# Optimization experiments

Hardware: AMD Instinct MI355X
Metric: run time of the kernel (lower is better)

The kernel has to match this reference:

```python
import jax, jax.numpy as jnp
import numpy as np

NFEAT, NHID, NHEADS = 512, 64, 8
ALPHA = 0.2
NEG = -9e15  # torch uses -9000000000000000.0


def _xavier(key, shape, gain=1.414):
    fan_in, fan_out = shape[-2], shape[-1]
    bound = gain * np.sqrt(6.0 / (fan_in + fan_out))
    return jax.random.uniform(key, shape, jnp.float32, -bound, bound)


def setup_inputs() -> dict:
    key = jax.random.key(0)
    ks = jax.random.split(key, 6)
    N = 2048
    x = jax.random.normal(ks[0], (N, NFEAT), jnp.float32)
    adj = jax.random.randint(ks[1], (N, N), 0, 2, jnp.int32)
    # per-head stacked params for the two attention banks
    W1 = _xavier(ks[2], (NHEADS, NFEAT, NHID))
    a1 = _xavier(ks[3], (NHEADS, 2 * NHID, 1))
    W2 = _xavier(ks[4], (NHEADS, NFEAT, NHID))
    a2 = _xavier(ks[5], (NHEADS, 2 * NHID, 1))
    return {"x": x, "adj": adj, "W1": W1, "a1": a1, "W2": W2, "a2": a2}


def _gat_bank(x, adj_mask, W, a):
    """All heads of one GraphAttentionLayer bank, vectorized over heads.
    x: [N, F], W: [H, F, O], a: [H, 2O, 1]. Returns concat output [N, H*O]
    and attention [H, N, N]."""
    N = x.shape[0]
    Wh = jnp.einsum('nf,hfo->hno', x, W)               # [H, N, O]
    a_src = a[:, :NHID, 0]                             # [H, O]
    a_dst = a[:, NHID:, 0]                             # [H, O]
    Wh1 = jnp.einsum('hno,ho->hn', Wh, a_src)          # [H, N]
    Wh2 = jnp.einsum('hno,ho->hn', Wh, a_dst)          # [H, N]
    e = Wh1[:, :, None] + Wh2[:, None, :]              # [H, N, N]
    e = jnp.where(e > 0, e, ALPHA * e)                 # LeakyReLU
    e = jnp.where(adj_mask[None, :, :], e, NEG)
    attention = jax.nn.softmax(e, axis=-1)             # [H, N, N]
    h_prime = jnp.einsum('hnm,hmo->hno', attention, Wh)
    out = jax.nn.elu(h_prime)                          # concat=True -> elu
    # torch.cat over heads along feature dim: [N, H*O]
    out = jnp.transpose(out, (1, 0, 2)).reshape(N, NHEADS * NHID)
    return out, attention


def reference(x, adj, W1, a1, W2, a2):
    adj_mask = adj > 0
    # dropout layers are no-ops in eval mode
    h1, att1 = _gat_bank(x, adj_mask, W1, a1)
    h1 = jax.nn.elu(h1)
    h2, att2 = _gat_bank(h1, adj_mask, W2, a2)
    h2 = jax.nn.elu(h2)
    return h2, att1, att2
```

## Files before the change

kernel.cpp:

```cpp
#include <hip/hip_runtime.h>
#include <hip/hip_bf16.h>


typedef __attribute__((ext_vector_type(8))) short bf16x8;
typedef __attribute__((ext_vector_type(4))) float f32x4;

__device__ __forceinline__ float bf2f(unsigned short u) {
    return __uint_as_float(((unsigned int)u) << 16);
}
__device__ __forceinline__ unsigned short f2bf(float f) {
    __hip_bfloat16 h = __float2bfloat16(f);
    return __builtin_bit_cast(unsigned short, h);
}
__device__ __forceinline__ float elu1(float x) { return x > 0.f ? x : expm1f(x); }

__global__ __launch_bounds__(256) void adjbits_kernel(
    const int* __restrict__ adj, unsigned long long* __restrict__ gbits) {
    int g = blockIdx.x * 256 + threadIdx.x;
    unsigned long long m = __ballot(adj[g] > 0);
    if ((threadIdx.x & 63) == 0) gbits[g >> 6] = m;
}

__global__ __launch_bounds__(256) void reorder_w_kernel(
    const float* __restrict__ W, unsigned short* __restrict__ WpHi,
    unsigned short* __restrict__ WpLo) {
    int i = blockIdx.x * 256 + threadIdx.x;
    int o = i & 63;
    int k = (i >> 6) & 511;
    int h = i >> 15;
    float v = W[i];
    unsigned short hi = f2bf(v);
    unsigned short lo = f2bf(v - bf2f(hi));
    long idx = (((h * 16) + (k >> 5)) * 64 + o) * 32 + (k & 31);
    WpHi[idx] = hi;
    WpLo[idx] = lo;
}

__global__ __launch_bounds__(256, 2) void gemm1_kernel(
    const float* __restrict__ A,
    const unsigned short* __restrict__ BpHi, const unsigned short* __restrict__ BpLo,
    const float* __restrict__ avec,
    unsigned short* __restrict__ Whp, float* __restrict__ s1, float* __restrict__ s2) {
    __shared__ float accred[2][64][20];
    const int bx   = blockIdx.x;
    const int h    = bx >> 6;
    const int mt   = bx & 63;
    const int tid  = threadIdx.x;
    const int wave = tid >> 6;
    const int lane = tid & 63;
    const int quad = lane >> 4;
    const int m16  = lane & 15;
    const int rw   = wave & 1;
    const int kw   = wave >> 1;
    const int rowbase = mt * 32 + rw * 16;

    const float* Arow = A + (long)(rowbase + m16) * 512 + kw * 256 + quad * 8;
    const long boff = ((long)(h * 16 + kw * 8) * 64 + m16) * 32 + quad * 8;
    const unsigned short* BH = BpHi + boff;
    const unsigned short* BL = BpLo + boff;

    f32x4 acc[4];
#pragma unroll
    for (int t = 0; t < 4; ++t)
#pragma unroll
        for (int r = 0; r < 4; ++r) acc[t][r] = 0.f;

    for (int kb = 0; kb < 8; ++kb) {
        const float* ap = Arow + kb * 32;
        bf16x8 ahi, alo;
#pragma unroll
        for (int j = 0; j < 8; ++j) {
            float v = ap[j];
            unsigned short hv = f2bf(v);
            ahi[j] = (short)hv;
            alo[j] = (short)f2bf(v - bf2f(hv));
        }
        const unsigned short* bh0 = BH + (long)kb * 2048;
        const unsigned short* bl0 = BL + (long)kb * 2048;
#pragma unroll
        for (int t = 0; t < 4; ++t) {
            bf16x8 bh = *reinterpret_cast<const bf16x8*>(bh0 + t * 512);
            bf16x8 bl = *reinterpret_cast<const bf16x8*>(bl0 + t * 512);
            acc[t] = __builtin_amdgcn_mfma_f32_16x16x32_bf16(alo, bh, acc[t], 0, 0, 0);
            acc[t] = __builtin_amdgcn_mfma_f32_16x16x32_bf16(ahi, bl, acc[t], 0, 0, 0);
            acc[t] = __builtin_amdgcn_mfma_f32_16x16x32_bf16(ahi, bh, acc[t], 0, 0, 0);
        }
    }

    if (kw == 1) {
#pragma unroll
        for (int t = 0; t < 4; ++t)
            *reinterpret_cast<f32x4*>(&accred[rw][t * 16 + m16][quad * 4]) = acc[t];
    }
    __syncthreads();
    if (kw == 1) return;

#pragma unroll
    for (int t = 0; t < 4; ++t) {
        f32x4 o = *reinterpret_cast<const f32x4*>(&accred[rw][t * 16 + m16][quad * 4]);
#pragma unroll
        for (int r = 0; r < 4; ++r) acc[t][r] += o[r];
    }

    float aS[4], aD[4];
#pragma unroll
    for (int t = 0; t < 4; ++t) {
        aS[t] = avec[(h << 7) + t * 16 + m16];
        aD[t] = avec[(h << 7) + 64 + t * 16 + m16];
    }
#pragma unroll
    for (int r = 0; r < 4; ++r) {
        float t1 = 0.f, t2 = 0.f;
#pragma unroll
        for (int t = 0; t < 4; ++t) {
            float v = acc[t][r];
            t1 = fmaf(v, aS[t], t1);
            t2 = fmaf(v, aD[t], t2);
        }
#pragma unroll
        for (int off = 1; off < 16; off <<= 1) {
            t1 += __shfl_xor(t1, off);
            t2 += __shfl_xor(t2, off);
        }
        if (m16 == 0) {
            int row = rowbase + quad * 4 + r;
            s1[(h << 11) + row] = t1;
            s2[(h << 11) + row] = t2;
        }
    }

#pragma unroll
    for (int t = 0; t < 4; ++t) {
        const int col = t * 16 + m16;
#pragma unroll
        for (int r = 0; r < 4; ++r) {
            const int row = rowbase + quad * 4 + r;
            long idx = (((long)(h * 64 + (row >> 5)) * 64 + col) << 5) + (row & 31);
            Whp[idx] = f2bf(acc[t][r]);
        }
    }
}

__global__ __launch_bounds__(256, 4) void fused_att_kernel(
    const float* __restrict__ s1g, const float* __restrict__ s2g,
    const unsigned int* __restrict__ gbits,
    const unsigned short* __restrict__ Whp,
    float* __restrict__ att, float* __restrict__ hout) {
    __shared__ unsigned int lbits[16 * 65];
    __shared__ float ls2[2048];
    __shared__ float lmax[4][16];
    __shared__ float lsum[4][16];
    __shared__ float accred[3][64][20];
    __shared__ f32x4 pstage[4][16][9];

    const int bx   = blockIdx.x;
    const int h    = bx >> 7;
    const int row0 = (bx & 127) << 4;
    const int tid  = threadIdx.x;
    const int wq   = tid >> 6;
    const int lane = tid & 63;
    const int quad = lane >> 4;
    const int m16  = lane & 15;

#pragma unroll
    for (int i = 0; i < 4; ++i) {
        int idx = i * 256 + tid;
        lbits[(idx >> 6) * 65 + (idx & 63)] = gbits[((row0 + (idx >> 6)) << 6) + (idx & 63)];
    }
    const float4* s2v4 = reinterpret_cast<const float4*>(s2g + (h << 11));
#pragma unroll
    for (int i = 0; i < 2; ++i) {
        int idx = i * 256 + tid;
        reinterpret_cast<float4*>(ls2)[idx] = s2v4[idx];
    }
    __syncthreads();

    const float s1i = s1g[(h << 11) + row0 + m16];

    float mx = -INFINITY;
    float lp = 0.f;
    for (int i = 0; i < 16; ++i) {
        const int jt = i * 4 + wq;
        unsigned int word = lbits[m16 * 65 + jt] >> (quad * 8);
        float4 sa = *reinterpret_cast<const float4*>(ls2 + jt * 32 + quad * 8);
        float4 sb = *reinterpret_cast<const float4*>(ls2 + jt * 32 + quad * 8 + 4);
        float sv[8] = {sa.x, sa.y, sa.z, sa.w, sb.x, sb.y, sb.z, sb.w};
        float ev[8];
        float bm = -INFINITY;
#pragma unroll
        for (int u = 0; u < 8; ++u) {
            float e = s1i + sv[u];
            e = fmaxf(e, 0.2f * e);
            ev[u] = e;
            bm = fmaxf(bm, ((word >> u) & 1u) ? e : -INFINITY);
        }
        float nm = fmaxf(mx, bm);
        float sc = (mx == nm) ? 1.f : __expf(mx - nm);
        lp *= sc;
        mx = nm;
#pragma unroll
        for (int u = 0; u < 8; ++u)
            lp += ((word >> u) & 1u) ? __expf(ev[u] - mx) : 0.f;
    }
#pragma unroll
    for (int off = 16; off < 64; off <<= 1) {
        float omx = __shfl_xor(mx, off);
        float olp = __shfl_xor(lp, off);
        float nm = fmaxf(mx, omx);
        float sa = (mx == nm) ? 1.f : __expf(mx - nm);
        float sb = (omx == nm) ? 1.f : __expf(omx - nm);
        lp = fmaf(lp, sa, olp * sb);
        mx = nm;
    }
    if (lane < 16) {
        lmax[wq][m16] = mx;
        lsum[wq][m16] = lp;
    }
    __syncthreads();
    float m = fmaxf(fmaxf(lmax[0][m16], lmax[1][m16]),
                    fmaxf(lmax[2][m16], lmax[3][m16]));
    float l = 0.f;
#pragma unroll
    for (int w = 0; w < 4; ++w) {
        float wm = lmax[w][m16];
        float ws = (wm == m) ? 1.f : __expf(wm - m);
        l = fmaf(lsum[w][m16], ws, l);
    }
    const bool am = (m == -INFINITY);
    const float invl = am ? 0.f : 1.f / l;
    const float fallb = 1.f / 2048.f;

    f32x4 acc[4];
#pragma unroll
    for (int t = 0; t < 4; ++t)
#pragma unroll
        for (int r = 0; r < 4; ++r) acc[t][r] = 0.f;

    const unsigned short* BW = Whp + ((long)(h << 12) + m16) * 32 + quad * 8;
    float* attbase = att + (long)h * 4194304 + (long)row0 * 2048;
    const int fr = lane >> 3;
    const int fc = lane & 7;

    for (int i = 0; i < 16; ++i) {
        const int jt = i * 4 + wq;
        unsigned int word = lbits[m16 * 65 + jt];
        float4 sa = *reinterpret_cast<const float4*>(ls2 + jt * 32 + quad * 8);
        float4 sb = *reinterpret_cast<const float4*>(ls2 + jt * 32 + quad * 8 + 4);
        float sv[8] = {sa.x, sa.y, sa.z, sa.w, sb.x, sb.y, sb.z, sb.w};
        float p[8];
        bf16x8 af;
#pragma unroll
        for (int u = 0; u < 8; ++u) {
            float e = s1i + sv[u];
            e = fmaxf(e, 0.2f * e);
            float pv = ((word >> (quad * 8 + u)) & 1u) ? __expf(e - m) * invl : 0.f;
            p[u] = am ? fallb : pv;
            af[u] = (short)f2bf(p[u]);
        }
        f32x4 plo, phi;
        plo[0] = p[0]; plo[1] = p[1]; plo[2] = p[2]; plo[3] = p[3];
        phi[0] = p[4]; phi[1] = p[5]; phi[2] = p[6]; phi[3] = p[7];
        pstage[wq][m16][quad * 2]     = plo;
        pstage[wq][m16][quad * 2 + 1] = phi;

        const unsigned short* b0 = BW + (long)jt * 2048;
#pragma unroll
        for (int t = 0; t < 4; ++t) {
            bf16x8 bf = *reinterpret_cast<const bf16x8*>(b0 + t * 512);
            acc[t] = __builtin_amdgcn_mfma_f32_16x16x32_bf16(af, bf, acc[t], 0, 0, 0);
        }

#pragma unroll
        for (int half = 0; half < 2; ++half) {
            const int r = half * 8 + fr;
            f32x4 v = pstage[wq][r][fc];
            __builtin_nontemporal_store(
                v, reinterpret_cast<f32x4*>(attbase + (long)r * 2048 + jt * 32 + fc * 4));
        }
    }

    if (wq > 0) {
#pragma unroll
        for (int t = 0; t < 4; ++t)
            *reinterpret_cast<f32x4*>(&accred[wq - 1][t * 16 + m16][quad * 4]) = acc[t];
    }
    __syncthreads();
    if (wq == 0) {
#pragma unroll
        for (int t = 0; t < 4; ++t) {
            const int col = t * 16 + m16;
#pragma unroll
            for (int w = 0; w < 3; ++w) {
                f32x4 o = *reinterpret_cast<const f32x4*>(&accred[w][col][quad * 4]);
#pragma unroll
                for (int r = 0; r < 4; ++r) acc[t][r] += o[r];
            }
#pragma unroll
            for (int r = 0; r < 4; ++r) {
                const int row = row0 + quad * 4 + r;
                hout[(row << 9) + (h << 6) + col] = elu1(elu1(acc[t][r]));
            }
        }
    }
}

extern "C" void kernel_launch(void* const* d_in, const int* in_sizes, int n_in,
                              void* d_out, int out_size, void* d_ws, size_t ws_size,
                              hipStream_t stream) {
    const float* x  = (const float*)d_in[0];
    const int* adj  = (const int*)d_in[1];
    const float* W1 = (const float*)d_in[2];
    const float* a1 = (const float*)d_in[3];
    const float* W2 = (const float*)d_in[4];
    const float* a2 = (const float*)d_in[5];

    float* out  = (float*)d_out;
    float* att1 = out + 1048576;
    float* att2 = att1 + 33554432;

    char* w = (char*)d_ws;
    unsigned short* WpHi1 = (unsigned short*)(w);
    unsigned short* WpLo1 = (unsigned short*)(w + 524288);
    unsigned short* WpHi2 = (unsigned short*)(w + 1048576);
    unsigned short* WpLo2 = (unsigned short*)(w + 1572864);
    unsigned short* Whp   = (unsigned short*)(w + 2097152);
    float* s1             = (float*)(w + 4194304);
    float* s2             = (float*)(w + 4259840);
    unsigned long long* gbits = (unsigned long long*)(w + 4325376);
    float* x2             = (float*)(w + 4849664);

    const unsigned int* gbits32 = (const unsigned int*)gbits;

    adjbits_kernel<<<16384, 256, 0, stream>>>(adj, gbits);
    reorder_w_kernel<<<1024, 256, 0, stream>>>(W1, WpHi1, WpLo1);
    reorder_w_kernel<<<1024, 256, 0, stream>>>(W2, WpHi2, WpLo2);

    gemm1_kernel<<<512, 256, 0, stream>>>(x, WpHi1, WpLo1, a1, Whp, s1, s2);
    fused_att_kernel<<<1024, 256, 0, stream>>>(s1, s2, gbits32, Whp, att1, x2);

    gemm1_kernel<<<512, 256, 0, stream>>>(x2, WpHi2, WpLo2, a2, Whp, s1, s2);
    fused_att_kernel<<<1024, 256, 0, stream>>>(s1, s2, gbits32, Whp, att2, out);
}
```

Before: 360.3 us.

## Stage attention tiles block-wide to emit full 1KB contiguous row stores

Each block now has all four waves write their probability tiles for eight column tiles (256 columns) into one shared staging buffer. After a barrier, the whole block writes contiguous 1 KB row segments of the attention matrix, replacing the per-wave 128-byte fragments. The staging buffer shares shared memory with the reduction scratch. The aim is better write coalescing on the dominant attention output traffic, paid for with two block-wide barriers per outer iteration that can stall the interleaved MFMA work.

```diff
diff --git a/kernel.cpp b/kernel.cpp
--- a/kernel.cpp
+++ b/kernel.cpp
@@ -150,8 +150,9 @@
     __shared__ float ls2[2048];
     __shared__ float lmax[4][16];
     __shared__ float lsum[4][16];
-    __shared__ float accred[3][64][20];
-    __shared__ f32x4 pstage[4][16][9];
+    __shared__ __align__(16) char upool[17152];
+    f32x4 (*pst)[67]      = reinterpret_cast<f32x4(*)[67]>(upool);
+    float (*accred)[64][20] = reinterpret_cast<float(*)[64][20]>(upool);
 
     const int bx   = blockIdx.x;
     const int h    = bx >> 7;
@@ -238,45 +239,50 @@
 
     const unsigned short* BW = Whp + ((long)(h << 12) + m16) * 32 + quad * 8;
     float* attbase = att + (long)h * 4194304 + (long)row0 * 2048;
-    const int fr = lane >> 3;
-    const int fc = lane & 7;
-
-    for (int i = 0; i < 16; ++i) {
-        const int jt = i * 4 + wq;
-        unsigned int word = lbits[m16 * 65 + jt];
-        float4 sa = *reinterpret_cast<const float4*>(ls2 + jt * 32 + quad * 8);
-        float4 sb = *reinterpret_cast<const float4*>(ls2 + jt * 32 + quad * 8 + 4);
-        float sv[8] = {sa.x, sa.y, sa.z, sa.w, sb.x, sb.y, sb.z, sb.w};
-        float p[8];
-        bf16x8 af;
-#pragma unroll
-        for (int u = 0; u < 8; ++u) {
-            float e = s1i + sv[u];
-            e = fmaxf(e, 0.2f * e);
-            float pv = ((word >> (quad * 8 + u)) & 1u) ? __expf(e - m) * invl : 0.f;
-            p[u] = am ? fallb : pv;
-            af[u] = (short)f2bf(p[u]);
-        }
-        f32x4 plo, phi;
-        plo[0] = p[0]; plo[1] = p[1]; plo[2] = p[2]; plo[3] = p[3];
-        phi[0] = p[4]; phi[1] = p[5]; phi[2] = p[6]; phi[3] = p[7];
-        pstage[wq][m16][quad * 2]     = plo;
-        pstage[wq][m16][quad * 2 + 1] = phi;
-
-        const unsigned short* b0 = BW + (long)jt * 2048;
-#pragma unroll
-        for (int t = 0; t < 4; ++t) {
-            bf16x8 bf = *reinterpret_cast<const bf16x8*>(b0 + t * 512);
-            acc[t] = __builtin_amdgcn_mfma_f32_16x16x32_bf16(af, bf, acc[t], 0, 0, 0);
-        }
-
-#pragma unroll
-        for (int half = 0; half < 2; ++half) {
-            const int r = half * 8 + fr;
-            f32x4 v = pstage[wq][r][fc];
+
+    for (int w8 = 0; w8 < 8; ++w8) {
+#pragma unroll
+        for (int p = 0; p < 2; ++p) {
+            const int jt = w8 * 8 + p * 4 + wq;
+            unsigned int word = lbits[m16 * 65 + jt];
+            float4 sa = *reinterpret_cast<const float4*>(ls2 + jt * 32 + quad * 8);
+            float4 sb = *reinterpret_cast<const float4*>(ls2 + jt * 32 + quad * 8 + 4);
+            float sv[8] = {sa.x, sa.y, sa.z, sa.w, sb.x, sb.y, sb.z, sb.w};
+            float pp[8];
+            bf16x8 af;
+#pragma unroll
+            for (int u = 0; u < 8; ++u) {
+                float e = s1i + sv[u];
+                e = fmaxf(e, 0.2f * e);
+                float pv = ((word >> (quad * 8 + u)) & 1u) ? __expf(e - m) * invl : 0.f;
+                pp[u] = am ? fallb : pv;
+                af[u] = (short)f2bf(pp[u]);
+            }
+            f32x4 plo, phi;
+            plo[0] = pp[0]; plo[1] = pp[1]; plo[2] = pp[2]; plo[3] = pp[3];
+            phi[0] = pp[4]; phi[1] = pp[5]; phi[2] = pp[6]; phi[3] = pp[7];
+            const int ub = (p * 4 + wq) * 8 + quad * 2;
+            pst[m16][ub]     = plo;
+            pst[m16][ub + 1] = phi;
+
+            const unsigned short* b0 = BW + (long)jt * 2048;
+#pragma unroll
+            for (int t = 0; t < 4; ++t) {
+                bf16x8 bf = *reinterpret_cast<const bf16x8*>(b0 + t * 512);
+                acc[t] = __builtin_amdgcn_mfma_f32_16x16x32_bf16(af, bf, acc[t], 0, 0, 0);
+            }
+        }
+        __syncthreads();
+        float* afb = attbase + w8 * 256;
+#pragma unroll
+        for (int s = 0; s < 4; ++s) {
+            int g = s * 256 + tid;
+            int r = g >> 6;
+            int u = g & 63;
             __builtin_nontemporal_store(
-                v, reinterpret_cast<f32x4*>(attbase + (long)r * 2048 + jt * 32 + fc * 4));
-        }
+                pst[r][u], reinterpret_cast<f32x4*>(afb + (long)r * 2048 + u * 4));
+        }
+        __syncthreads();
     }
 
     if (wq > 0) {
```

After: 365.4 us. Within noise of the previous version (+1.4%).

## Split fused attention into softmax-stats and attention-PV kernels

Applied to the files above, without the earlier changes.

The fused attention kernel is split in two. One kernel computes the per-row softmax max and inverse sum and writes them to a workspace buffer. A second kernel recomputes the logits, writes the attention matrix and does the P·V MFMA. The second kernel aliases its staging and reduction shared memory into one pool to raise occupancy, and changes its column-tile order from interleaved across waves to contiguous per wave. The cost is an extra launch, an extra pass over the bitmask and s2 per block, and a round trip of the stats through global memory.

```diff
diff --git a/kernel.cpp b/kernel.cpp
--- a/kernel.cpp
+++ b/kernel.cpp
@@ -141,17 +141,13 @@
     }
 }
 
-__global__ __launch_bounds__(256, 4) void fused_att_kernel(
+__global__ __launch_bounds__(256, 4) void softmax_stats_kernel(
     const float* __restrict__ s1g, const float* __restrict__ s2g,
-    const unsigned int* __restrict__ gbits,
-    const unsigned short* __restrict__ Whp,
-    float* __restrict__ att, float* __restrict__ hout) {
+    const unsigned int* __restrict__ gbits, float2* __restrict__ mrow) {
     __shared__ unsigned int lbits[16 * 65];
     __shared__ float ls2[2048];
     __shared__ float lmax[4][16];
     __shared__ float lsum[4][16];
-    __shared__ float accred[3][64][20];
-    __shared__ f32x4 pstage[4][16][9];
 
     const int bx   = blockIdx.x;
     const int h    = bx >> 7;
@@ -217,17 +213,63 @@
         lsum[wq][m16] = lp;
     }
     __syncthreads();
-    float m = fmaxf(fmaxf(lmax[0][m16], lmax[1][m16]),
-                    fmaxf(lmax[2][m16], lmax[3][m16]));
-    float l = 0.f;
-#pragma unroll
-    for (int w = 0; w < 4; ++w) {
-        float wm = lmax[w][m16];
-        float ws = (wm == m) ? 1.f : __expf(wm - m);
-        l = fmaf(lsum[w][m16], ws, l);
-    }
+    if (wq == 0 && lane < 16) {
+        float m = fmaxf(fmaxf(lmax[0][m16], lmax[1][m16]),
+                        fmaxf(lmax[2][m16], lmax[3][m16]));
+        float l = 0.f;
+#pragma unroll
+        for (int w = 0; w < 4; ++w) {
+            float wm = lmax[w][m16];
+            float ws = (wm == m) ? 1.f : __expf(wm - m);
+            l = fmaf(lsum[w][m16], ws, l);
+        }
+        const bool am = (m == -INFINITY);
+        float2 o;
+        o.x = m;
+        o.y = am ? 0.f : 1.f / l;
+        mrow[(h << 11) + row0 + m16] = o;
+    }
+}
+
+__global__ __launch_bounds__(256, 4) void att_pv_kernel(
+    const float* __restrict__ s1g, const float* __restrict__ s2g,
+    const unsigned int* __restrict__ gbits,
+    const unsigned short* __restrict__ Whp,
+    const float2* __restrict__ mrow,
+    float* __restrict__ att, float* __restrict__ hout) {
+    __shared__ unsigned int lbits[16 * 65];
+    __shared__ float ls2[2048];
+    __shared__ __align__(16) char upool[15360];
+    f32x4 (*pstage)[16][9]  = reinterpret_cast<f32x4(*)[16][9]>(upool);
+    float (*accred)[64][20] = reinterpret_cast<float(*)[64][20]>(upool);
+
+    const int bx   = blockIdx.x;
+    const int h    = bx >> 7;
+    const int row0 = (bx & 127) << 4;
+    const int tid  = threadIdx.x;
+    const int wq   = tid >> 6;
+    const int lane = tid & 63;
+    const int quad = lane >> 4;
+    const int m16  = lane & 15;
+
+#pragma unroll
+    for (int i = 0; i < 4; ++i) {
+        int idx = i * 256 + tid;
+        lbits[(idx >> 6) * 65 + (idx & 63)] = gbits[((row0 + (idx >> 6)) << 6) + (idx & 63)];
+    }
+    const float4* s2v4 = reinterpret_cast<const float4*>(s2g + (h << 11));
+#pragma unroll
+    for (int i = 0; i < 2; ++i) {
+        int idx = i * 256 + tid;
+        reinterpret_cast<float4*>(ls2)[idx] = s2v4[idx];
+    }
+    __syncthreads();
+
+    const float s1i = s1g[(h << 11) + row0 + m16];
+    const float2 mi = mrow[(h << 11) + row0 + m16];
+    const float m = mi.x;
+    const float invl = mi.y;
     const bool am = (m == -INFINITY);
-    const float invl = am ? 0.f : 1.f / l;
     const float fallb = 1.f / 2048.f;
 
     f32x4 acc[4];
@@ -242,7 +284,7 @@
     const int fc = lane & 7;
 
     for (int i = 0; i < 16; ++i) {
-        const int jt = i * 4 + wq;
+        const int jt = wq * 16 + i;
         unsigned int word = lbits[m16 * 65 + jt];
         float4 sa = *reinterpret_cast<const float4*>(ls2 + jt * 32 + quad * 8);
         float4 sb = *reinterpret_cast<const float4*>(ls2 + jt * 32 + quad * 8 + 4);
@@ -279,6 +321,7 @@
         }
     }
 
+    __syncthreads();
     if (wq > 0) {
 #pragma unroll
         for (int t = 0; t < 4; ++t)
@@ -328,6 +371,7 @@
     float* s2             = (float*)(w + 4259840);
     unsigned long long* gbits = (unsigned long long*)(w + 4325376);
     float* x2             = (float*)(w + 4849664);
+    float2* mrow          = (float2*)(w + 9043968);
 
     const unsigned int* gbits32 = (const unsigned int*)gbits;
 
@@ -336,8 +380,10 @@
     reorder_w_kernel<<<1024, 256, 0, stream>>>(W2, WpHi2, WpLo2);
 
     gemm1_kernel<<<512, 256, 0, stream>>>(x, WpHi1, WpLo1, a1, Whp, s1, s2);
-    fused_att_kernel<<<1024, 256, 0, stream>>>(s1, s2, gbits32, Whp, att1, x2);
+    softmax_stats_kernel<<<1024, 256, 0, stream>>>(s1, s2, gbits32, mrow);
+    att_pv_kernel<<<1024, 256, 0, stream>>>(s1, s2, gbits32, Whp, mrow, att1, x2);
 
     gemm1_kernel<<<512, 256, 0, stream>>>(x2, WpHi2, WpLo2, a2, Whp, s1, s2);
-    fused_att_kernel<<<1024, 256, 0, stream>>>(s1, s2, gbits32, Whp, att2, out);
-}
+    softmax_stats_kernel<<<1024, 256, 0, stream>>>(s1, s2, gbits32, mrow);
+    att_pv_kernel<<<1024, 256, 0, stream>>>(s1, s2, gbits32, Whp, mrow, att2, out);
+}
```

Result: slower. 378.3 us (+5.0%).

## Merge all GAT stages into one persistent kernel with grid barriers

Applied to the files above, without the earlier changes.

Replaces the seven separate launches (adjacency bit-packing, two weight reorders, two GEMMs, two fused attention passes) with one 1024-block persistent kernel whose phases are separated by atomic-counter grid barriers. The GEMM phase now gives each block 16 rows with a four-way K split reduced through shared memory, and the attention loop gives each wave a contiguous range of column tiles instead of an interleaved one. The aim is to remove per-launch overhead and inter-kernel gaps. The barrier assumes all 1024 blocks are co-resident (4 per CU on 256 CUs) and has a spin limit that could silently let a phase proceed too early.

```diff
diff --git a/kernel.cpp b/kernel.cpp
--- a/kernel.cpp
+++ b/kernel.cpp
@@ -14,48 +14,41 @@
 }
 __device__ __forceinline__ float elu1(float x) { return x > 0.f ? x : expm1f(x); }
 
-__global__ __launch_bounds__(256) void adjbits_kernel(
-    const int* __restrict__ adj, unsigned long long* __restrict__ gbits) {
-    int g = blockIdx.x * 256 + threadIdx.x;
-    unsigned long long m = __ballot(adj[g] > 0);
-    if ((threadIdx.x & 63) == 0) gbits[g >> 6] = m;
-}
-
-__global__ __launch_bounds__(256) void reorder_w_kernel(
-    const float* __restrict__ W, unsigned short* __restrict__ WpHi,
-    unsigned short* __restrict__ WpLo) {
-    int i = blockIdx.x * 256 + threadIdx.x;
-    int o = i & 63;
-    int k = (i >> 6) & 511;
-    int h = i >> 15;
-    float v = W[i];
-    unsigned short hi = f2bf(v);
-    unsigned short lo = f2bf(v - bf2f(hi));
-    long idx = (((h * 16) + (k >> 5)) * 64 + o) * 32 + (k & 31);
-    WpHi[idx] = hi;
-    WpLo[idx] = lo;
-}
-
-__global__ __launch_bounds__(256, 2) void gemm1_kernel(
+__device__ __forceinline__ void gridbar(unsigned* cnt, unsigned target) {
+    __syncthreads();
+    if (threadIdx.x == 0) {
+        __threadfence();
+        atomicAdd(cnt, 1u);
+        long spin = 0;
+        while (atomicAdd(cnt, 0u) < target && spin < (1L << 22)) {
+            __builtin_amdgcn_s_sleep(2);
+            ++spin;
+        }
+        __threadfence();
+    }
+    __syncthreads();
+}
+
+__global__ void init_cnt_kernel(unsigned* cnt) { *cnt = 0u; }
+
+
+__device__ __forceinline__ void gemm_phase(
+    char* pool, int bx, int tid,
     const float* __restrict__ A,
     const unsigned short* __restrict__ BpHi, const unsigned short* __restrict__ BpLo,
     const float* __restrict__ avec,
     unsigned short* __restrict__ Whp, float* __restrict__ s1, float* __restrict__ s2) {
-    __shared__ float accred[2][64][20];
-    const int bx   = blockIdx.x;
-    const int h    = bx >> 6;
-    const int mt   = bx & 63;
-    const int tid  = threadIdx.x;
+    float (*accredG)[64][20] = reinterpret_cast<float(*)[64][20]>(pool);
+    const int h    = bx >> 7;
+    const int mt   = bx & 127;
     const int wave = tid >> 6;
     const int lane = tid & 63;
     const int quad = lane >> 4;
     const int m16  = lane & 15;
-    const int rw   = wave & 1;
-    const int kw   = wave >> 1;
-    const int rowbase = mt * 32 + rw * 16;
-
-    const float* Arow = A + (long)(rowbase + m16) * 512 + kw * 256 + quad * 8;
-    const long boff = ((long)(h * 16 + kw * 8) * 64 + m16) * 32 + quad * 8;
+    const int rowbase = mt * 16;
+
+    const float* Arow = A + (long)(rowbase + m16) * 512 + wave * 128 + quad * 8;
+    const long boff = ((long)(h * 16 + wave * 4) * 64 + m16) * 32 + quad * 8;
     const unsigned short* BH = BpHi + boff;
     const unsigned short* BL = BpLo + boff;
 
@@ -65,7 +58,8 @@
 #pragma unroll
         for (int r = 0; r < 4; ++r) acc[t][r] = 0.f;
 
-    for (int kb = 0; kb < 8; ++kb) {
+#pragma unroll
+    for (int kb = 0; kb < 4; ++kb) {
         const float* ap = Arow + kb * 32;
         bf16x8 ahi, alo;
 #pragma unroll
@@ -87,20 +81,20 @@
         }
     }
 
-    if (kw == 1) {
-#pragma unroll
-        for (int t = 0; t < 4; ++t)
-            *reinterpret_cast<f32x4*>(&accred[rw][t * 16 + m16][quad * 4]) = acc[t];
-    }
-    __syncthreads();
-    if (kw == 1) return;
-
-#pragma unroll
-    for (int t = 0; t < 4; ++t) {
-        f32x4 o = *reinterpret_cast<const f32x4*>(&accred[rw][t * 16 + m16][quad * 4]);
-#pragma unroll
-        for (int r = 0; r < 4; ++r) acc[t][r] += o[r];
-    }
+#pragma unroll
+    for (int t = 0; t < 4; ++t)
+        *reinterpret_cast<f32x4*>(&accredG[wave][t * 16 + m16][quad * 4]) = acc[t];
+    __syncthreads();
+    if (wave != 0) return;
+
+#pragma unroll
+    for (int w = 1; w < 4; ++w)
+#pragma unroll
+        for (int t = 0; t < 4; ++t) {
+            f32x4 o = *reinterpret_cast<const f32x4*>(&accredG[w][t * 16 + m16][quad * 4]);
+#pragma unroll
+            for (int r = 0; r < 4; ++r) acc[t][r] += o[r];
+        }
 
     float aS[4], aD[4];
 #pragma unroll
@@ -141,22 +135,21 @@
     }
 }
 
-__global__ __launch_bounds__(256, 4) void fused_att_kernel(
+__device__ __forceinline__ void fused_phase(
+    char* pool, int bx, int tid,
     const float* __restrict__ s1g, const float* __restrict__ s2g,
     const unsigned int* __restrict__ gbits,
     const unsigned short* __restrict__ Whp,
     float* __restrict__ att, float* __restrict__ hout) {
-    __shared__ unsigned int lbits[16 * 65];
-    __shared__ float ls2[2048];
-    __shared__ float lmax[4][16];
-    __shared__ float lsum[4][16];
-    __shared__ float accred[3][64][20];
-    __shared__ f32x4 pstage[4][16][9];
-
-    const int bx   = blockIdx.x;
+    unsigned int* lbits = reinterpret_cast<unsigned int*>(pool);
+    float* ls2          = reinterpret_cast<float*>(pool + 4160);
+    float (*lmax)[16]   = reinterpret_cast<float(*)[16]>(pool + 12352);
+    float (*lsum)[16]   = reinterpret_cast<float(*)[16]>(pool + 12608);
+    f32x4 (*pstage)[16][9]  = reinterpret_cast<f32x4(*)[16][9]>(pool + 12864);
+    float (*accredF)[64][20] = reinterpret_cast<float(*)[64][20]>(pool + 12864);
+
     const int h    = bx >> 7;
     const int row0 = (bx & 127) << 4;
-    const int tid  = threadIdx.x;
     const int wq   = tid >> 6;
     const int lane = tid & 63;
     const int quad = lane >> 4;
@@ -180,7 +173,7 @@
     float mx = -INFINITY;
     float lp = 0.f;
     for (int i = 0; i < 16; ++i) {
-        const int jt = i * 4 + wq;
+        const int jt = wq * 16 + i;
         unsigned int word = lbits[m16 * 65 + jt] >> (quad * 8);
         float4 sa = *reinterpret_cast<const float4*>(ls2 + jt * 32 + quad * 8);
         float4 sb = *reinterpret_cast<const float4*>(ls2 + jt * 32 + quad * 8 + 4);
@@ -242,7 +235,7 @@
     const int fc = lane & 7;
 
     for (int i = 0; i < 16; ++i) {
-        const int jt = i * 4 + wq;
+        const int jt = wq * 16 + i;
         unsigned int word = lbits[m16 * 65 + jt];
         float4 sa = *reinterpret_cast<const float4*>(ls2 + jt * 32 + quad * 8);
         float4 sb = *reinterpret_cast<const float4*>(ls2 + jt * 32 + quad * 8 + 4);
@@ -279,10 +272,11 @@
         }
     }
 
+    __syncthreads();
     if (wq > 0) {
 #pragma unroll
         for (int t = 0; t < 4; ++t)
-            *reinterpret_cast<f32x4*>(&accred[wq - 1][t * 16 + m16][quad * 4]) = acc[t];
+            *reinterpret_cast<f32x4*>(&accredF[wq - 1][t * 16 + m16][quad * 4]) = acc[t];
     }
     __syncthreads();
     if (wq == 0) {
@@ -291,7 +285,7 @@
             const int col = t * 16 + m16;
 #pragma unroll
             for (int w = 0; w < 3; ++w) {
-                f32x4 o = *reinterpret_cast<const f32x4*>(&accred[w][col][quad * 4]);
+                f32x4 o = *reinterpret_cast<const f32x4*>(&accredF[w][col][quad * 4]);
 #pragma unroll
                 for (int r = 0; r < 4; ++r) acc[t][r] += o[r];
             }
@@ -302,6 +296,55 @@
             }
         }
     }
+}
+
+__global__ __launch_bounds__(256, 4) void gat_persistent(
+    const float* __restrict__ x, const int* __restrict__ adj,
+    const float* __restrict__ W1, const float* __restrict__ a1,
+    const float* __restrict__ W2, const float* __restrict__ a2,
+    float* __restrict__ out, float* __restrict__ att1, float* __restrict__ att2,
+    unsigned short* __restrict__ Wp1Hi, unsigned short* __restrict__ Wp1Lo,
+    unsigned short* __restrict__ Wp2Hi, unsigned short* __restrict__ Wp2Lo,
+    unsigned short* __restrict__ Whp, float* __restrict__ s1, float* __restrict__ s2,
+    unsigned long long* __restrict__ gbits, float* __restrict__ x2,
+    unsigned* __restrict__ cnt) {
+    __shared__ __align__(16) char pool[28224];
+    const int bx  = blockIdx.x;
+    const int tid = threadIdx.x;
+
+#pragma unroll
+    for (int i = 0; i < 16; ++i) {
+        int g = bx * 4096 + i * 256 + tid;
+        unsigned long long mb = __ballot(adj[g] > 0);
+        if ((tid & 63) == 0) gbits[g >> 6] = mb;
+    }
+    {
+        int idx = bx * 256 + tid;
+        int o = idx & 63;
+        int k = (idx >> 6) & 511;
+        int h = idx >> 15;
+        long widx = (((h * 16) + (k >> 5)) * 64 + o) * 32 + (k & 31);
+        float v1 = W1[idx];
+        unsigned short h1 = f2bf(v1);
+        Wp1Hi[widx] = h1;
+        Wp1Lo[widx] = f2bf(v1 - bf2f(h1));
+        float v2 = W2[idx];
+        unsigned short h2 = f2bf(v2);
+        Wp2Hi[widx] = h2;
+        Wp2Lo[widx] = f2bf(v2 - bf2f(h2));
+    }
+    gridbar(cnt, 1024);
+
+    const unsigned int* gbits32 = (const unsigned int*)gbits;
+
+    gemm_phase(pool, bx, tid, x, Wp1Hi, Wp1Lo, a1, Whp, s1, s2);
+    gridbar(cnt, 2048);
+    fused_phase(pool, bx, tid, s1, s2, gbits32, Whp, att1, x2);
+    gridbar(cnt, 3072);
+
+    gemm_phase(pool, bx, tid, x2, Wp2Hi, Wp2Lo, a2, Whp, s1, s2);
+    gridbar(cnt, 4096);
+    fused_phase(pool, bx, tid, s1, s2, gbits32, Whp, att2, out);
 }
 
 extern "C" void kernel_launch(void* const* d_in, const int* in_sizes, int n_in,
@@ -319,25 +362,19 @@
     float* att2 = att1 + 33554432;
 
     char* w = (char*)d_ws;
-    unsigned short* WpHi1 = (unsigned short*)(w);
-    unsigned short* WpLo1 = (unsigned short*)(w + 524288);
-    unsigned short* WpHi2 = (unsigned short*)(w + 1048576);
-    unsigned short* WpLo2 = (unsigned short*)(w + 1572864);
+    unsigned short* Wp1Hi = (unsigned short*)(w);
+    unsigned short* Wp1Lo = (unsigned short*)(w + 524288);
+    unsigned short* Wp2Hi = (unsigned short*)(w + 1048576);
+    unsigned short* Wp2Lo = (unsigned short*)(w + 1572864);
     unsigned short* Whp   = (unsigned short*)(w + 2097152);
     float* s1             = (float*)(w + 4194304);
     float* s2             = (float*)(w + 4259840);
     unsigned long long* gbits = (unsigned long long*)(w + 4325376);
     float* x2             = (float*)(w + 4849664);
-
-    const unsigned int* gbits32 = (const unsigned int*)gbits;
-
-    adjbits_kernel<<<16384, 256, 0, stream>>>(adj, gbits);
-    reorder_w_kernel<<<1024, 256, 0, stream>>>(W1, WpHi1, WpLo1);
-    reorder_w_kernel<<<1024, 256, 0, stream>>>(W2, WpHi2, WpLo2);
-
-    gemm1_kernel<<<512, 256, 0, stream>>>(x, WpHi1, WpLo1, a1, Whp, s1, s2);
-    fused_att_kernel<<<1024, 256, 0, stream>>>(s1, s2, gbits32, Whp, att1, x2);
-
-    gemm1_kernel<<<512, 256, 0, stream>>>(x2, WpHi2, WpLo2, a2, Whp, s1, s2);
-    fused_att_kernel<<<1024, 256, 0, stream>>>(s1, s2, gbits32, Whp, att2, out);
-}
+    unsigned* cnt         = (unsigned*)(w + 9043968);
+
+    init_cnt_kernel<<<1, 1, 0, stream>>>(cnt);
+    gat_persistent<<<1024, 256, 0, stream>>>(
+        x, adj, W1, a1, W2, a2, out, att1, att2,
+        Wp1Hi, Wp1Lo, Wp2Hi, Wp2Lo, Whp, s1, s2, gbits, x2, cnt);
+}
```

After: 824.6 us. +128.9%, slower.
